# Kernel optimization log

Hardware: AMD Instinct MI355X
Metric: run time of the kernel (lower is better)

## Reference

```python
import jax, jax.numpy as jnp
import numpy as np
from jax import lax

M_POINT = 1024
NSAMPLE = 16
GRASPNESS_THRESHOLD = 0.1
HMIN, HMAX = -0.02, 0.04  # cylinder height range (GraspNet CloudCrop)
RADII = (0.025, 0.05, 0.075, 0.1)
BIG = 1e10


def _fps(xyz, mask):
    """Masked furthest point sampling. xyz [N,3], mask [N] bool -> idx [M_POINT] int32.
    Masked-out points carry -BIG min-distance so they are never selected."""
    first = jnp.argmax(mask).astype(jnp.int32)  # first graspable point (ragged FPS start)
    dists = jnp.where(mask, BIG, -BIG)
    idxs = jnp.zeros((M_POINT,), jnp.int32).at[0].set(first)

    def body(i, carry):
        idxs, dists = carry
        last = xyz[idxs[i - 1]]
        d = jnp.sum((xyz - last) ** 2, axis=-1)
        dists = jnp.where(mask, jnp.minimum(dists, d), -BIG)
        nxt = jnp.argmax(dists).astype(jnp.int32)
        return idxs.at[i].set(nxt), dists

    idxs, _ = lax.fori_loop(1, M_POINT, body, (idxs, dists))
    return idxs


def _cylinder_crop(xyz_g, feat_g, rot, radius, w1, b1, w2, b2):
    """Cylinder query + group + shared MLP + maxpool.
    xyz_g [B,M,3], feat_g [B,M,C], rot [B,M,3,3] -> [B,M,256]."""
    B, M, _ = xyz_g.shape
    # offsets of candidate n relative to seed m, expressed in the seed's gripper frame
    diff = xyz_g[:, None, :, :] - xyz_g[:, :, None, :]          # [B,M(seed),M(cand),3]
    local = jnp.einsum('bmnj,bmji->bmni', diff, rot)            # rotate into approach frame
    along = local[..., 0]
    r2 = local[..., 1] ** 2 + local[..., 2] ** 2
    cond = (r2 < radius * radius) & (along > HMIN) & (along < HMAX)  # [B,M,M]
    # first NSAMPLE in-cylinder indices (ball-query semantics: pad with first hit)
    order = jnp.where(cond, jnp.arange(M)[None, None, :], M)
    sel = jnp.argsort(order, axis=-1)[..., :NSAMPLE].astype(jnp.int32)  # [B,M,NS]
    cnt = cond.sum(axis=-1)                                     # [B,M]
    fill = sel[..., :1]
    idx = jnp.where(jnp.arange(NSAMPLE)[None, None, :] < cnt[..., None], sel, fill)
    idx = jnp.where(cnt[..., None] > 0, idx, 0)
    grouped_xyz = jnp.take_along_axis(local, idx[..., None], axis=2) / radius  # [B,M,NS,3]
    grouped_feat = feat_g[jnp.arange(B)[:, None, None], idx]                    # [B,M,NS,C]
    g = jnp.concatenate([grouped_xyz, grouped_feat], axis=-1)                   # [B,M,NS,3+C]
    h = jax.nn.relu(jnp.einsum('bmnf,of->bmno', g, w1) + b1)
    h = jax.nn.relu(jnp.einsum('bmnf,of->bmno', h, w2) + b2)
    return h.max(axis=2)                                                        # [B,M,256]


def setup_inputs() -> dict:
    key = jax.random.key(0)
    ks = jax.random.split(key, 10)
    B, N, C = 4, 20000, 512
    return {
        'seed_xyz': jax.random.normal(ks[0], (B, N, 3), jnp.float32),
        'seed_features': jax.random.normal(ks[1], (B, C, N), jnp.float32),
        'objectness_score': jax.random.normal(ks[2], (B, 2, N), jnp.float32),
        'graspness_score': jax.random.uniform(ks[3], (B, N), jnp.float32),
        'grasp_top_views_rot': jax.random.normal(ks[4], (B, M_POINT, 3, 3), jnp.float32),
        'crop_w1': jax.random.normal(ks[5], (4, 256, 3 + C), jnp.float32) * 0.05,
        'crop_b1': jnp.zeros((4, 256), jnp.float32),
        'crop_w2': jax.random.normal(ks[6], (4, 256, 256), jnp.float32) * 0.05,
        'crop_b2': jnp.zeros((4, 256), jnp.float32),
        'fuse_w': jax.random.normal(ks[7], (256, 1024), jnp.float32) * 0.05,
        'fuse_b': jnp.zeros((256,), jnp.float32),
    }


def reference(seed_xyz, seed_features, objectness_score, graspness_score,
              grasp_top_views_rot, crop_w1, crop_b1, crop_w2, crop_b2,
              fuse_w, fuse_b):
    # graspable mask (per-point, data dependent)
    objectness_mask = jnp.argmax(objectness_score, axis=1) == 1       # [B,N]
    graspness_mask = graspness_score > GRASPNESS_THRESHOLD
    graspable_mask = objectness_mask & graspness_mask
    # masked FPS per sample, then gather
    idxs = jax.vmap(_fps)(seed_xyz, graspable_mask)                    # [B,M]
    xyz_g = jnp.take_along_axis(seed_xyz, idxs[:, :, None], axis=1)    # [B,M,3]
    feat = seed_features.transpose(0, 2, 1)                            # [B,N,C]
    feat_g = jnp.take_along_axis(feat, idxs[:, :, None], axis=1)       # [B,M,C]
    # multiscale cylinder crops
    feats = [_cylinder_crop(xyz_g, feat_g, grasp_top_views_rot, RADII[k],
                            crop_w1[k], crop_b1[k], crop_w2[k], crop_b2[k])
             for k in range(4)]
    cat = jnp.concatenate(feats, axis=-1)                              # [B,M,1024]
    fused = jnp.einsum('bmf,of->bom', cat, fuse_w) + fuse_b[None, :, None]  # [B,256,M]
    return fused
```

## Files before the change

### kernel.cpp

```cpp
#include <hip/hip_runtime.h>
#include <cstdint>
#include <cfloat>
#include <climits>

#define NPTS 20000
#define NB 4
#define MP 1024
#define CF 512
#define MAXCH 20
#define KFAST 10240
#define PPAIR 10

__constant__ float c_r2[4]  = { (float)(0.025*0.025), (float)(0.05*0.05),
                                (float)(0.075*0.075), (float)(0.1*0.1) };
__constant__ float c_rad[4] = { 0.025f, 0.05f, 0.075f, 0.1f };

#define DPP_XOR1   0xB1
#define DPP_XOR2   0x4E
#define DPP_HMIRR  0x141
#define DPP_MIRR   0x140
#define DPP_BC15   0x142
#define DPP_BC31   0x143

typedef float v2f __attribute__((ext_vector_type(2)));

__device__ __forceinline__ v2f pk_add(v2f a, v2f b){
    v2f d; asm("v_pk_add_f32 %0, %1, %2" : "=v"(d) : "v"(a), "v"(b)); return d;
}
__device__ __forceinline__ v2f pk_mul(v2f a, v2f b){
    v2f d; asm("v_pk_mul_f32 %0, %1, %2" : "=v"(d) : "v"(a), "v"(b)); return d;
}

template<int CTRL>
__device__ __forceinline__ float fmax_dpp(float m)
{
    int mi = __float_as_int(m);
    int oi = __builtin_amdgcn_update_dpp(mi, mi, CTRL, 0xf, 0xf, false);
    return fmaxf(m, __int_as_float(oi));
}

template<int CTRL>
__device__ __forceinline__ unsigned long long kmax_step(unsigned long long k)
{
    unsigned int lo = (unsigned int)k;
    unsigned int hi = (unsigned int)(k >> 32);
    unsigned int olo = (unsigned int)__builtin_amdgcn_update_dpp((int)lo, (int)lo, CTRL, 0xf, 0xf, false);
    unsigned int ohi = (unsigned int)__builtin_amdgcn_update_dpp((int)hi, (int)hi, CTRL, 0xf, 0xf, false);
    unsigned long long ok = ((unsigned long long)ohi << 32) | (unsigned long long)olo;
    return (ok > k) ? ok : k;
}

__global__ __launch_bounds__(1024)
void k_fps_compact(const float* __restrict__ xyz, const float* __restrict__ obj,
                   const float* __restrict__ grasp,
                   float* __restrict__ xc, float* __restrict__ yc,
                   float* __restrict__ zc, int* __restrict__ ci,
                   int* __restrict__ kv)
{
    const int b = blockIdx.x;
    const int tid = threadIdx.x;
    const int lane = tid & 63, wid = tid >> 6;
    const float* xb  = xyz   + (size_t)b * NPTS * 3;
    const float* ob0 = obj   + (size_t)b * 2 * NPTS;
    const float* ob1 = ob0 + NPTS;
    const float* gb  = grasp + (size_t)b * NPTS;
    float* xcb = xc + (size_t)b * 20480;
    float* ycb = yc + (size_t)b * 20480;
    float* zcb = zc + (size_t)b * 20480;
    int*   cib = ci + (size_t)b * 20480;

    __shared__ int sWaveCnt[16];

    int kbase = 0;
    for (int i = 0; i < MAXCH; ++i) {
        int n = i * MP + tid;
        bool msk = false; float x = 0.f, y = 0.f, z = 0.f;
        if (n < NPTS) {
            msk = (ob1[n] > ob0[n]) && (gb[n] > 0.1f);
            if (msk) { x = xb[n*3+0]; y = xb[n*3+1]; z = xb[n*3+2]; }
        }
        unsigned long long bal = __ballot(msk);
        if (lane == 0) sWaveCnt[wid] = __popcll(bal);
        __syncthreads();
        int pre = 0, tot = 0;
        for (int w = 0; w < 16; ++w) { int c = sWaveCnt[w]; tot += c; if (w < wid) pre += c; }
        if (msk) {
            int rank = kbase + pre + __popcll(bal & ((1ull << lane) - 1ull));
            xcb[rank] = x; ycb[rank] = y; zcb[rank] = z; cib[rank] = n;
        }
        kbase += tot;
        __syncthreads();
    }
    if (tid == 0) kv[b] = kbase;
}

__global__ __launch_bounds__(512, 2)
void k_fps_loop(const float* __restrict__ xyz, const int* __restrict__ kv,
                const float* __restrict__ xc, const float* __restrict__ yc,
                const float* __restrict__ zc, const int* __restrict__ ci,
                int* __restrict__ idxs, float* __restrict__ xyz_g)
{
    const int b = blockIdx.x;
    const int tid = threadIdx.x;
    const int lane = tid & 63, wid = tid >> 6;
    const float* xb  = xyz + (size_t)b * NPTS * 3;
    const float* xcb = xc + (size_t)b * 20480;
    const float* ycb = yc + (size_t)b * 20480;
    const float* zcb = zc + (size_t)b * 20480;
    const int*   cib = ci + (size_t)b * 20480;

    __shared__ float sXYZ[3 * KFAST];
    __shared__ int   s_sel[MP];
    __shared__ unsigned long long sKy[2][8];
    __shared__ float sMax[2][8];
    __shared__ int   sWinc[2];
    float* sX = sXYZ;
    float* sY = sXYZ + KFAST;
    float* sZ = sXYZ + 2 * KFAST;

    const int K = kv[b];

    if (K == 0) {
        for (int t = tid; t < MP; t += 512) {
            idxs[b*MP + t] = 0;
            xyz_g[((size_t)b*MP + t)*3 + 0] = xb[0];
            xyz_g[((size_t)b*MP + t)*3 + 1] = xb[1];
            xyz_g[((size_t)b*MP + t)*3 + 2] = xb[2];
        }
        return;
    }

    if (K <= KFAST) {
        for (int c = tid; c < KFAST; c += 512) {
            bool v = c < K;
            sX[c] = v ? xcb[c] : 0.f;
            sY[c] = v ? ycb[c] : 0.f;
            sZ[c] = v ? zcb[c] : 0.f;
        }
        if (tid == 0) { s_sel[0] = 0; sWinc[0] = 0x7fffffff; sWinc[1] = 0x7fffffff; }
        __syncthreads();

        v2f px2[PPAIR], py2[PPAIR], pz2[PPAIR], pd2[PPAIR];
#pragma unroll
        for (int i = 0; i < PPAIR; ++i) {
            int c0 = tid + ((2*i) << 9);
            int c1 = c0 + 512;
            px2[i].x = sX[c0]; px2[i].y = sX[c1];
            py2[i].x = sY[c0]; py2[i].y = sY[c1];
            pz2[i].x = sZ[c0]; pz2[i].y = sZ[c1];
            pd2[i].x = (c0 < K) ? 1e10f : -3.0e38f;
            pd2[i].y = (c1 < K) ? 1e10f : -3.0e38f;
            asm volatile("" : "+v"(px2[i]), "+v"(py2[i]), "+v"(pz2[i]));
        }
        v2f nlx2, nly2, nlz2;
        {
            float lx = sX[0], ly = sY[0], lz = sZ[0];
            nlx2.x = nlx2.y = -lx; nly2.x = nly2.y = -ly; nlz2.x = nlz2.y = -lz;
        }

        for (int it = 1; it < MP; ++it) {
            const int p = it & 1;
#pragma unroll
            for (int i = 0; i < PPAIR; ++i) {
                v2f dx = pk_add(px2[i], nlx2);
                v2f dy = pk_add(py2[i], nly2);
                v2f dz = pk_add(pz2[i], nlz2);
                v2f s  = pk_add(pk_add(pk_mul(dx,dx), pk_mul(dy,dy)), pk_mul(dz,dz));
                pd2[i].x = fminf(pd2[i].x, s.x);
                pd2[i].y = fminf(pd2[i].y, s.y);
            }
            float q0 = fmaxf(pd2[0].x, pd2[0].y);
            float q1 = fmaxf(pd2[1].x, pd2[1].y);
            float q2 = fmaxf(pd2[2].x, pd2[2].y);
            float q3 = fmaxf(pd2[3].x, pd2[3].y);
            float q4 = fmaxf(pd2[4].x, pd2[4].y);
            float q5 = fmaxf(pd2[5].x, pd2[5].y);
            float q6 = fmaxf(pd2[6].x, pd2[6].y);
            float q7 = fmaxf(pd2[7].x, pd2[7].y);
            float q8 = fmaxf(pd2[8].x, pd2[8].y);
            float q9 = fmaxf(pd2[9].x, pd2[9].y);
            float r0 = fmaxf(fmaxf(q0, q1), fmaxf(q2, q3));
            float r1 = fmaxf(fmaxf(q4, q5), fmaxf(q6, q7));
            float bv = fmaxf(fmaxf(r0, r1), fmaxf(q8, q9));

            float wm = bv;
            wm = fmax_dpp<DPP_XOR1 >(wm);
            wm = fmax_dpp<DPP_XOR2 >(wm);
            wm = fmax_dpp<DPP_HMIRR>(wm);
            wm = fmax_dpp<DPP_MIRR >(wm);
            wm = fmax_dpp<DPP_BC15 >(wm);
            wm = fmax_dpp<DPP_BC31 >(wm);
            if (lane == 63) sMax[p][wid] = wm;
            __syncthreads();
            float g = sMax[p][lane & 7];
            g = fmax_dpp<DPP_XOR1 >(g);
            g = fmax_dpp<DPP_XOR2 >(g);
            g = fmax_dpp<DPP_HMIRR>(g);
            if (tid == 0) sWinc[p ^ 1] = 0x7fffffff;
            if (bv == g) {
                int c = 0x7fffffff;
#pragma unroll
                for (int i = PPAIR - 1; i >= 0; --i) {
                    if (pd2[i].y == g) c = tid + ((2*i+1) << 9);
                    if (pd2[i].x == g) c = tid + ((2*i  ) << 9);
                }
                atomicMin(&sWinc[p], c);
            }
            __syncthreads();
            int n = sWinc[p];
            if (tid == 0) s_sel[it] = n;
            float nx = sX[n], ny = sY[n], nz = sZ[n];
            nlx2.x = nlx2.y = -nx;
            nly2.x = nly2.y = -ny;
            nlz2.x = nlz2.y = -nz;
        }
        __syncthreads();
        for (int t = tid; t < MP; t += 512) {
            int nc = s_sel[t];
            idxs[b*MP + t] = cib[nc];
            xyz_g[((size_t)b*MP + t)*3 + 0] = sX[nc];
            xyz_g[((size_t)b*MP + t)*3 + 1] = sY[nc];
            xyz_g[((size_t)b*MP + t)*3 + 2] = sZ[nc];
        }
        return;
    }

    {
        float* fD = sXYZ;
        for (int c = tid; c < K; c += 512) fD[c] = 1e10f;
        float lx = xcb[0], ly = ycb[0], lz = zcb[0];
        if (tid == 0) s_sel[0] = 0;
        __syncthreads();
        for (int it = 1; it < MP; ++it) {
            const int p = it & 1;
            float bv = -3.4e38f; int bn = 0;
            for (int c = tid; c < K; c += 512) {
                float dx = xcb[c] - lx, dy = ycb[c] - ly, dz = zcb[c] - lz;
                float d = __fadd_rn(__fadd_rn(__fmul_rn(dx,dx), __fmul_rn(dy,dy)),
                                    __fmul_rn(dz,dz));
                float nd = fminf(fD[c], d);
                fD[c] = nd;
                bool w = nd > bv;
                bn = w ? c : bn;
                bv = fmaxf(bv, nd);
            }
            unsigned int ob = __float_as_uint(bv);
            unsigned int ord = (ob & 0x80000000u) ? ~ob : (ob | 0x80000000u);
            unsigned long long key = ((unsigned long long)ord << 32)
                                   | (unsigned int)(~bn);
            key = kmax_step<DPP_XOR1 >(key);
            key = kmax_step<DPP_XOR2 >(key);
            key = kmax_step<DPP_HMIRR>(key);
            key = kmax_step<DPP_MIRR >(key);
            key = kmax_step<DPP_BC15 >(key);
            key = kmax_step<DPP_BC31 >(key);
            if (lane == 63) sKy[p][wid] = key;
            __syncthreads();
            unsigned long long k2 = sKy[p][lane & 7];
            k2 = kmax_step<DPP_XOR1 >(k2);
            k2 = kmax_step<DPP_XOR2 >(k2);
            k2 = kmax_step<DPP_HMIRR>(k2);
            int n = ~((unsigned int)k2);
            lx = xcb[n]; ly = ycb[n]; lz = zcb[n];
            if (tid == 0) s_sel[it] = n;
        }
        __syncthreads();
        for (int t = tid; t < MP; t += 512) {
            int nc = s_sel[t];
            idxs[b*MP + t] = cib[nc];
            xyz_g[((size_t)b*MP + t)*3 + 0] = xcb[nc];
            xyz_g[((size_t)b*MP + t)*3 + 1] = ycb[nc];
            xyz_g[((size_t)b*MP + t)*3 + 2] = zcb[nc];
        }
    }
}

__global__ void k_gather_feat(const float* __restrict__ sf, const int* __restrict__ idxs,
                              float* __restrict__ feat_g)
{
    int bm = blockIdx.x;
    int b = bm >> 10;
    int n = idxs[bm];
    const float* src = sf + (size_t)b*CF*NPTS + n;
    float* dst = feat_g + (size_t)bm*CF;
    for (int c = threadIdx.x; c < CF; c += 256) dst[c] = src[(size_t)c * NPTS];
}

__global__ void k_prep(const float* __restrict__ w1, const float* __restrict__ w2,
                       float* __restrict__ w2t, float* __restrict__ w1x)
{
    int k = blockIdx.x, cb = blockIdx.y*32, ob = blockIdx.z*32;
    int tx = threadIdx.x & 31, ty = threadIdx.x >> 5;
    __shared__ float t[32][33];
    for (int r = ty; r < 32; r += 8)
        t[r][tx] = w2[((size_t)k*256 + ob + r)*256 + cb + tx];
    __syncthreads();
    for (int r = ty; r < 32; r += 8)
        w2t[((size_t)k*256 + cb + r)*256 + ob + tx] = t[tx][r];
    if (blockIdx.y == 0 && blockIdx.z == 0) {
        int o = threadIdx.x;
        for (int d = 0; d < 3; ++d)
            w1x[(k*3 + d)*256 + o] = w1[((size_t)k*256 + o)*515 + d];
    }
}

__global__ __launch_bounds__(256)
void k_f1(const float* __restrict__ feat_g, const float* __restrict__ w1,
          const float* __restrict__ b1, float* __restrict__ F1)
{
    const int rt = blockIdx.x * 64;
    const int ot = blockIdx.y * 64;
    const int k  = blockIdx.z;
    const int tid = threadIdx.x;
    __shared__ float As[16][68];
    __shared__ float Bs[16][68];
    const int lr = tid >> 2;
    const int lc = (tid & 3) * 4;
    const int tr = (tid & 15) * 4;
    const int tc = (tid >> 4) * 4;
    float acc[4][4] = {};
    for (int kk = 0; kk < CF; kk += 16) {
        const float* ap = feat_g + (size_t)(rt + lr)*CF + kk + lc;
        As[lc+0][lr] = ap[0]; As[lc+1][lr] = ap[1];
        As[lc+2][lr] = ap[2]; As[lc+3][lr] = ap[3];
        const float* bp = w1 + (size_t)(k*256 + ot + lr)*515 + 3 + kk + lc;
        Bs[lc+0][lr] = bp[0]; Bs[lc+1][lr] = bp[1];
        Bs[lc+2][lr] = bp[2]; Bs[lc+3][lr] = bp[3];
        __syncthreads();
#pragma unroll
        for (int cc = 0; cc < 16; ++cc) {
            float a0=As[cc][tr+0], a1=As[cc][tr+1], a2=As[cc][tr+2], a3=As[cc][tr+3];
            float q0=Bs[cc][tc+0], q1=Bs[cc][tc+1], q2=Bs[cc][tc+2], q3=Bs[cc][tc+3];
            acc[0][0]+=a0*q0; acc[0][1]+=a0*q1; acc[0][2]+=a0*q2; acc[0][3]+=a0*q3;
            acc[1][0]+=a1*q0; acc[1][1]+=a1*q1; acc[1][2]+=a1*q2; acc[1][3]+=a1*q3;
            acc[2][0]+=a2*q0; acc[2][1]+=a2*q1; acc[2][2]+=a2*q2; acc[2][3]+=a2*q3;
            acc[3][0]+=a3*q0; acc[3][1]+=a3*q1; acc[3][2]+=a3*q2; acc[3][3]+=a3*q3;
        }
        __syncthreads();
    }
#pragma unroll
    for (int i = 0; i < 4; ++i)
#pragma unroll
        for (int j = 0; j < 4; ++j)
            F1[((size_t)k*4096 + rt+tr+i)*256 + ot+tc+j] = acc[i][j] + b1[k*256 + ot+tc+j];
}

__global__ __launch_bounds__(1024)
void k_nbr(const float* __restrict__ xyz_g, const float* __restrict__ rot,
           int* __restrict__ sel, float* __restrict__ lxyz, int* __restrict__ cnt)
{
    const int bm = blockIdx.x;
    const int b = bm >> 10;
    const int tid = threadIdx.x;
    const int lane = tid & 63, wid = tid >> 6;
    __shared__ float sR[9], sC[3];
    __shared__ int   sSel[4][16];
    __shared__ float sL[4][16][3];
    __shared__ int   sW[16];
    __shared__ int   sCnt[4];
    __shared__ float sFb[3];
    if (tid < 9) sR[tid] = rot[(size_t)bm*9 + tid];
    if (tid < 3) sC[tid] = xyz_g[(size_t)bm*3 + tid];
    __syncthreads();
    float x = xyz_g[((size_t)b*MP + tid)*3 + 0];
    float y = xyz_g[((size_t)b*MP + tid)*3 + 1];
    float z = xyz_g[((size_t)b*MP + tid)*3 + 2];
    float dx = x - sC[0], dy = y - sC[1], dz = z - sC[2];
    float l0 = __fadd_rn(__fadd_rn(__fmul_rn(dx,sR[0]), __fmul_rn(dy,sR[3])), __fmul_rn(dz,sR[6]));
    float l1 = __fadd_rn(__fadd_rn(__fmul_rn(dx,sR[1]), __fmul_rn(dy,sR[4])), __fmul_rn(dz,sR[7]));
    float l2 = __fadd_rn(__fadd_rn(__fmul_rn(dx,sR[2]), __fmul_rn(dy,sR[5])), __fmul_rn(dz,sR[8]));
    float r2 = __fadd_rn(__fmul_rn(l1,l1), __fmul_rn(l2,l2));
    bool basec = (l0 > -0.02f) && (l0 < 0.04f);
    if (tid == 0) { sFb[0]=l0; sFb[1]=l1; sFb[2]=l2; }
    for (int k = 0; k < 4; ++k) {
        bool c = basec && (r2 < c_r2[k]);
        unsigned long long bal = __ballot(c);
        if (lane == 0) sW[wid] = __popcll(bal);
        __syncthreads();
        int pre = 0, tot = 0;
        for (int w = 0; w < 16; ++w) { int cw = sW[w]; tot += cw; if (w < wid) pre += cw; }
        int rank = pre + __popcll(bal & ((1ull << lane) - 1ull));
        if (c && rank < 16) {
            sSel[k][rank] = tid;
            sL[k][rank][0] = l0; sL[k][rank][1] = l1; sL[k][rank][2] = l2;
        }
        if (tid == 0) sCnt[k] = min(tot, 16);
        __syncthreads();
    }
    if (tid < 64) {
        int k = tid >> 4, j = tid & 15;
        int ck = sCnt[k];
        int src = (j < ck) ? j : 0;
        int v; float a0, a1, a2;
        if (ck > 0) { v = sSel[k][src]; a0=sL[k][src][0]; a1=sL[k][src][1]; a2=sL[k][src][2]; }
        else        { v = 0; a0=sFb[0]; a1=sFb[1]; a2=sFb[2]; }
        size_t off = ((size_t)bm*4 + k)*16 + j;
        sel[off] = v;
        lxyz[off*3+0]=a0; lxyz[off*3+1]=a1; lxyz[off*3+2]=a2;
        if (j == 0) cnt[bm*4 + k] = (ck > 0) ? ck : 1;
    }
}

__global__ __launch_bounds__(256)
void k_mlp(const float* __restrict__ F1, const float* __restrict__ w1x,
           const float* __restrict__ w2t, const float* __restrict__ b2,
           const int* __restrict__ sel, const float* __restrict__ lxyz,
           const int* __restrict__ cnt, float* __restrict__ cat)
{
    const int gid = blockIdx.x;
    const int k = gid & 3;
    const int g0 = (gid >> 2) * 4;
    const int o = threadIdx.x;
    __shared__ float h1s[64][256];
    int u0 = cnt[(g0+0)*4 + k], u1 = cnt[(g0+1)*4 + k],
        u2 = cnt[(g0+2)*4 + k], u3 = cnt[(g0+3)*4 + k];
    int off1 = u0, off2 = u0+u1, off3 = off2+u2, tot = off3+u3;
    const float wx0 = w1x[(k*3+0)*256 + o];
    const float wx1 = w1x[(k*3+1)*256 + o];
    const float wx2 = w1x[(k*3+2)*256 + o];
    const float rad = c_rad[k];
    const int bbase = (g0 >> 10) * MP;
    for (int r = 0; r < tot; ++r) {
        int t = (r >= off1) + (r >= off2) + (r >= off3);
        int toff = (t==0) ? 0 : ((t==1) ? off1 : ((t==2) ? off2 : off3));
        int j = r - toff;
        int bmk = (g0 + t)*4 + k;
        int n = sel[(size_t)bmk*16 + j];
        float lx = lxyz[((size_t)bmk*16 + j)*3 + 0];
        float ly = lxyz[((size_t)bmk*16 + j)*3 + 1];
        float lz = lxyz[((size_t)bmk*16 + j)*3 + 2];
        float v = F1[((size_t)k*4096 + bbase + n)*256 + o];
        v += (lx/rad)*wx0 + (ly/rad)*wx1 + (lz/rad)*wx2;
        h1s[r][o] = fmaxf(v, 0.f);
    }
    __syncthreads();
    const float b2v = b2[k*256 + o];
    float m0=0.f, m1=0.f, m2=0.f, m3=0.f;
    const float* w2c = w2t + (size_t)k*65536 + o;
    for (int base = 0; base < tot; base += 4) {
        int r0 = base;
        int r1 = min(base+1, tot-1);
        int r2 = min(base+2, tot-1);
        int r3 = min(base+3, tot-1);
        float a0=0.f, a1=0.f, a2=0.f, a3=0.f;
        for (int c = 0; c < 256; c += 4) {
            float wA = w2c[(c+0)*256], wB = w2c[(c+1)*256];
            float wC = w2c[(c+2)*256], wD = w2c[(c+3)*256];
            float4 h;
            h = *(const float4*)&h1s[r0][c]; a0 += h.x*wA + h.y*wB + h.z*wC + h.w*wD;
            h = *(const float4*)&h1s[r1][c]; a1 += h.x*wA + h.y*wB + h.z*wC + h.w*wD;
            h = *(const float4*)&h1s[r2][c]; a2 += h.x*wA + h.y*wB + h.z*wC + h.w*wD;
            h = *(const float4*)&h1s[r3][c]; a3 += h.x*wA + h.y*wB + h.z*wC + h.w*wD;
        }
#pragma unroll
        for (int q = 0; q < 4; ++q) {
            int r = base + q;
            if (r < tot) {
                float a = (q==0) ? a0 : ((q==1) ? a1 : ((q==2) ? a2 : a3));
                int t = (r >= off1) + (r >= off2) + (r >= off3);
                float val = fmaxf(a + b2v, 0.f);
                if      (t==0) m0 = fmaxf(m0, val);
                else if (t==1) m1 = fmaxf(m1, val);
                else if (t==2) m2 = fmaxf(m2, val);
                else           m3 = fmaxf(m3, val);
            }
        }
    }
    cat[(size_t)(g0+0)*1024 + k*256 + o] = m0;
    cat[(size_t)(g0+1)*1024 + k*256 + o] = m1;
    cat[(size_t)(g0+2)*1024 + k*256 + o] = m2;
    cat[(size_t)(g0+3)*1024 + k*256 + o] = m3;
}

__global__ void k_transpose(const float* __restrict__ cat, float* __restrict__ catT)
{
    int bt = blockIdx.x;
    int b = bt >> 10;
    int t2 = bt & 1023;
    int mi = (t2 >> 5) * 32, fi = (t2 & 31) * 32;
    int tx = threadIdx.x & 31, ty = threadIdx.x >> 5;
    __shared__ float t[32][33];
    const float* src = cat + (size_t)b * 1048576;
    float* dst = catT + (size_t)b * 1048576;
    for (int r = ty; r < 32; r += 8) t[r][tx] = src[(size_t)(mi + r)*1024 + fi + tx];
    __syncthreads();
    for (int r = ty; r < 32; r += 8) dst[(size_t)(fi + r)*1024 + mi + tx] = t[tx][r];
}

__global__ __launch_bounds__(256)
void k_fuse(const float* __restrict__ catT, const float* __restrict__ fw,
            const float* __restrict__ fb, float* __restrict__ out)
{
    const int o0 = blockIdx.x * 4;
    const int b = blockIdx.y;
    const int m = threadIdx.x * 4;
    const float* ct = catT + (size_t)b * 1048576 + m;
    float4 a0 = {0,0,0,0}, a1 = a0, a2 = a0, a3 = a0;
    for (int f = 0; f < 1024; ++f) {
        const float4 cv = *(const float4*)(ct + (size_t)f*1024);
        float w0 = fw[(size_t)(o0+0)*1024 + f];
        float w1 = fw[(size_t)(o0+1)*1024 + f];
        float w2 = fw[(size_t)(o0+2)*1024 + f];
        float w3 = fw[(size_t)(o0+3)*1024 + f];
        a0.x += cv.x*w0; a0.y += cv.y*w0; a0.z += cv.z*w0; a0.w += cv.w*w0;
        a1.x += cv.x*w1; a1.y += cv.y*w1; a1.z += cv.z*w1; a1.w += cv.w*w1;
        a2.x += cv.x*w2; a2.y += cv.y*w2; a2.z += cv.z*w2; a2.w += cv.w*w2;
        a3.x += cv.x*w3; a3.y += cv.y*w3; a3.z += cv.z*w3; a3.w += cv.w*w3;
    }
#pragma unroll
    for (int q = 0; q < 4; ++q) {
        float bb = fb[o0+q];
        float4 r = (q==0) ? a0 : ((q==1) ? a1 : ((q==2) ? a2 : a3));
        r.x += bb; r.y += bb; r.z += bb; r.w += bb;
        *(float4*)&out[((size_t)b*256 + o0 + q)*1024 + m] = r;
    }
}

extern "C" void kernel_launch(void* const* d_in, const int* in_sizes, int n_in,
                              void* d_out, int out_size, void* d_ws, size_t ws_size,
                              hipStream_t stream)
{
    const float* seed_xyz      = (const float*)d_in[0];
    const float* seed_features = (const float*)d_in[1];
    const float* objectness    = (const float*)d_in[2];
    const float* graspness     = (const float*)d_in[3];
    const float* rot           = (const float*)d_in[4];
    const float* w1            = (const float*)d_in[5];
    const float* b1            = (const float*)d_in[6];
    const float* w2            = (const float*)d_in[7];
    const float* b2            = (const float*)d_in[8];
    const float* fw            = (const float*)d_in[9];
    const float* fb            = (const float*)d_in[10];
    float* out = (float*)d_out;

    char* ws = (char*)d_ws;
    size_t off = 0;
    int*   idxs   = (int*)(ws + off);  off += 16u<<10;
    float* xyz_g  = (float*)(ws + off); off += 48u<<10;
    float* feat_g = (float*)(ws + off); off += 8u<<20;
    float* F1     = (float*)(ws + off); off += 16u<<20;
    float* w2t    = (float*)(ws + off); off += 1u<<20;
    float* w1x    = (float*)(ws + off); off += 64u<<10;
    int*   sel    = (int*)(ws + off);   off += 1u<<20;
    int*   cnt    = (int*)(ws + off);   off += 64u<<10;
    float* lxyz   = (float*)(ws + off); off += 3u<<20;
    float* cat    = (float*)(ws + off); off += 16u<<20;
    float* catT   = (float*)(ws + off); off += 16u<<20;

    float* xc = cat;
    float* yc = cat + 4*20480;
    float* zc = cat + 8*20480;
    int*   ci = (int*)(cat + 12*20480);
    int*   kv = (int*)((char*)w1x + 32768);

    k_fps_compact<<<NB, 1024, 0, stream>>>(seed_xyz, objectness, graspness,
                                           xc, yc, zc, ci, kv);
    k_fps_loop<<<NB, 512, 0, stream>>>(seed_xyz, kv, xc, yc, zc, ci, idxs, xyz_g);
    k_prep<<<dim3(4,8,8), 256, 0, stream>>>(w1, w2, w2t, w1x);
    k_gather_feat<<<NB*MP, 256, 0, stream>>>(seed_features, idxs, feat_g);
    k_f1<<<dim3(64,4,4), 256, 0, stream>>>(feat_g, w1, b1, F1);
    k_nbr<<<NB*MP, 1024, 0, stream>>>(xyz_g, rot, sel, lxyz, cnt);
    k_mlp<<<4096, 256, 0, stream>>>(F1, w1x, w2t, b2, sel, lxyz, cnt, cat);
    k_transpose<<<4096, 256, 0, stream>>>(cat, catT);
    k_fuse<<<dim3(64,4), 256, 0, stream>>>(catT, fw, fb, out);
}
```

Baseline: 1.771 ms.

## Shrink FPS block to 256 threads and use single-barrier packed key argmax

The FPS loop kernel now runs with 256 threads per block, each holding 40 points in registers instead of 20. The per-iteration argmax is changed from a float max reduction, a barrier and a shared atomicMin tie-break followed by a second barrier, to one packed 64-bit (distance, ~index) key reduction across lanes with one barrier; every thread then reads the four wave keys directly. This removes a barrier and the atomic from each of the 1023 sequential iterations. In exchange each thread does twice the distance work and the block has fewer waves to hide latency, with more register pressure.

```diff
diff --git a/kernel.cpp b/kernel.cpp
--- a/kernel.cpp
+++ b/kernel.cpp
@@ -9,7 +9,8 @@
 #define CF 512
 #define MAXCH 20
 #define KFAST 10240
-#define PPAIR 10
+#define THR 256
+#define PPAIR 20
 
 __constant__ float c_r2[4]  = { (float)(0.025*0.025), (float)(0.05*0.05),
                                 (float)(0.075*0.075), (float)(0.1*0.1) };
@@ -29,14 +30,6 @@
 }
 __device__ __forceinline__ v2f pk_mul(v2f a, v2f b){
     v2f d; asm("v_pk_mul_f32 %0, %1, %2" : "=v"(d) : "v"(a), "v"(b)); return d;
-}
-
-template<int CTRL>
-__device__ __forceinline__ float fmax_dpp(float m)
-{
-    int mi = __float_as_int(m);
-    int oi = __builtin_amdgcn_update_dpp(mi, mi, CTRL, 0xf, 0xf, false);
-    return fmaxf(m, __int_as_float(oi));
 }
 
 template<int CTRL>
@@ -94,7 +87,7 @@
     if (tid == 0) kv[b] = kbase;
 }
 
-__global__ __launch_bounds__(512, 2)
+__global__ __launch_bounds__(256, 1)
 void k_fps_loop(const float* __restrict__ xyz, const int* __restrict__ kv,
                 const float* __restrict__ xc, const float* __restrict__ yc,
                 const float* __restrict__ zc, const int* __restrict__ ci,
@@ -111,9 +104,7 @@
 
     __shared__ float sXYZ[3 * KFAST];
     __shared__ int   s_sel[MP];
-    __shared__ unsigned long long sKy[2][8];
-    __shared__ float sMax[2][8];
-    __shared__ int   sWinc[2];
+    __shared__ unsigned long long sKy[2][4];
     float* sX = sXYZ;
     float* sY = sXYZ + KFAST;
     float* sZ = sXYZ + 2 * KFAST;
@@ -121,7 +112,7 @@
     const int K = kv[b];
 
     if (K == 0) {
-        for (int t = tid; t < MP; t += 512) {
+        for (int t = tid; t < MP; t += THR) {
             idxs[b*MP + t] = 0;
             xyz_g[((size_t)b*MP + t)*3 + 0] = xb[0];
             xyz_g[((size_t)b*MP + t)*3 + 1] = xb[1];
@@ -131,20 +122,20 @@
     }
 
     if (K <= KFAST) {
-        for (int c = tid; c < KFAST; c += 512) {
+        for (int c = tid; c < KFAST; c += THR) {
             bool v = c < K;
             sX[c] = v ? xcb[c] : 0.f;
             sY[c] = v ? ycb[c] : 0.f;
             sZ[c] = v ? zcb[c] : 0.f;
         }
-        if (tid == 0) { s_sel[0] = 0; sWinc[0] = 0x7fffffff; sWinc[1] = 0x7fffffff; }
+        if (tid == 0) s_sel[0] = 0;
         __syncthreads();
 
         v2f px2[PPAIR], py2[PPAIR], pz2[PPAIR], pd2[PPAIR];
 #pragma unroll
         for (int i = 0; i < PPAIR; ++i) {
-            int c0 = tid + ((2*i) << 9);
-            int c1 = c0 + 512;
+            int c0 = tid + ((2*i) << 8);
+            int c1 = c0 + THR;
             px2[i].x = sX[c0]; px2[i].y = sX[c1];
             py2[i].x = sY[c0]; py2[i].y = sY[c1];
             pz2[i].x = sZ[c0]; pz2[i].y = sZ[c1];
@@ -169,45 +160,39 @@
                 pd2[i].x = fminf(pd2[i].x, s.x);
                 pd2[i].y = fminf(pd2[i].y, s.y);
             }
-            float q0 = fmaxf(pd2[0].x, pd2[0].y);
-            float q1 = fmaxf(pd2[1].x, pd2[1].y);
-            float q2 = fmaxf(pd2[2].x, pd2[2].y);
-            float q3 = fmaxf(pd2[3].x, pd2[3].y);
-            float q4 = fmaxf(pd2[4].x, pd2[4].y);
-            float q5 = fmaxf(pd2[5].x, pd2[5].y);
-            float q6 = fmaxf(pd2[6].x, pd2[6].y);
-            float q7 = fmaxf(pd2[7].x, pd2[7].y);
-            float q8 = fmaxf(pd2[8].x, pd2[8].y);
-            float q9 = fmaxf(pd2[9].x, pd2[9].y);
-            float r0 = fmaxf(fmaxf(q0, q1), fmaxf(q2, q3));
-            float r1 = fmaxf(fmaxf(q4, q5), fmaxf(q6, q7));
-            float bv = fmaxf(fmaxf(r0, r1), fmaxf(q8, q9));
-
-            float wm = bv;
-            wm = fmax_dpp<DPP_XOR1 >(wm);
-            wm = fmax_dpp<DPP_XOR2 >(wm);
-            wm = fmax_dpp<DPP_HMIRR>(wm);
-            wm = fmax_dpp<DPP_MIRR >(wm);
-            wm = fmax_dpp<DPP_BC15 >(wm);
-            wm = fmax_dpp<DPP_BC31 >(wm);
-            if (lane == 63) sMax[p][wid] = wm;
+            float q[PPAIR];
+#pragma unroll
+            for (int i = 0; i < PPAIR; ++i) q[i] = fmaxf(pd2[i].x, pd2[i].y);
+            float t0 = fmaxf(fmaxf(q[0], q[1]),  fmaxf(q[2], q[3]));
+            float t1 = fmaxf(fmaxf(q[4], q[5]),  fmaxf(q[6], q[7]));
+            float t2 = fmaxf(fmaxf(q[8], q[9]),  fmaxf(q[10], q[11]));
+            float t3 = fmaxf(fmaxf(q[12], q[13]), fmaxf(q[14], q[15]));
+            float t4 = fmaxf(fmaxf(q[16], q[17]), fmaxf(q[18], q[19]));
+            float bv = fmaxf(fmaxf(fmaxf(t0, t1), fmaxf(t2, t3)), t4);
+            int c = 0x7fffffff;
+#pragma unroll
+            for (int i = PPAIR - 1; i >= 0; --i) {
+                if (pd2[i].y == bv) c = tid + ((2*i+1) << 8);
+                if (pd2[i].x == bv) c = tid + ((2*i  ) << 8);
+            }
+            unsigned int ob = __float_as_uint(bv);
+            unsigned int ord = (ob & 0x80000000u) ? ~ob : (ob | 0x80000000u);
+            unsigned long long key = ((unsigned long long)ord << 32)
+                                   | (unsigned int)(~c);
+            key = kmax_step<DPP_XOR1 >(key);
+            key = kmax_step<DPP_XOR2 >(key);
+            key = kmax_step<DPP_HMIRR>(key);
+            key = kmax_step<DPP_MIRR >(key);
+            key = kmax_step<DPP_BC15 >(key);
+            key = kmax_step<DPP_BC31 >(key);
+            if (lane == 63) sKy[p][wid] = key;
             __syncthreads();
-            float g = sMax[p][lane & 7];
-            g = fmax_dpp<DPP_XOR1 >(g);
-            g = fmax_dpp<DPP_XOR2 >(g);
-            g = fmax_dpp<DPP_HMIRR>(g);
-            if (tid == 0) sWinc[p ^ 1] = 0x7fffffff;
-            if (bv == g) {
-                int c = 0x7fffffff;
-#pragma unroll
-                for (int i = PPAIR - 1; i >= 0; --i) {
-                    if (pd2[i].y == g) c = tid + ((2*i+1) << 9);
-                    if (pd2[i].x == g) c = tid + ((2*i  ) << 9);
-                }
-                atomicMin(&sWinc[p], c);
-            }
-            __syncthreads();
-            int n = sWinc[p];
+            unsigned long long ka = sKy[p][0], kb = sKy[p][1];
+            unsigned long long kc = sKy[p][2], kd = sKy[p][3];
+            unsigned long long m01 = (kb > ka) ? kb : ka;
+            unsigned long long m23 = (kd > kc) ? kd : kc;
+            unsigned long long km  = (m23 > m01) ? m23 : m01;
+            int n = ~((unsigned int)km);
             if (tid == 0) s_sel[it] = n;
             float nx = sX[n], ny = sY[n], nz = sZ[n];
             nlx2.x = nlx2.y = -nx;
@@ -215,7 +200,7 @@
             nlz2.x = nlz2.y = -nz;
         }
         __syncthreads();
-        for (int t = tid; t < MP; t += 512) {
+        for (int t = tid; t < MP; t += THR) {
             int nc = s_sel[t];
             idxs[b*MP + t] = cib[nc];
             xyz_g[((size_t)b*MP + t)*3 + 0] = sX[nc];
@@ -227,14 +212,14 @@
 
     {
         float* fD = sXYZ;
-        for (int c = tid; c < K; c += 512) fD[c] = 1e10f;
+        for (int c = tid; c < K; c += THR) fD[c] = 1e10f;
         float lx = xcb[0], ly = ycb[0], lz = zcb[0];
         if (tid == 0) s_sel[0] = 0;
         __syncthreads();
         for (int it = 1; it < MP; ++it) {
             const int p = it & 1;
             float bv = -3.4e38f; int bn = 0;
-            for (int c = tid; c < K; c += 512) {
+            for (int c = tid; c < K; c += THR) {
                 float dx = xcb[c] - lx, dy = ycb[c] - ly, dz = zcb[c] - lz;
                 float d = __fadd_rn(__fadd_rn(__fmul_rn(dx,dx), __fmul_rn(dy,dy)),
                                     __fmul_rn(dz,dz));
@@ -256,16 +241,17 @@
             key = kmax_step<DPP_BC31 >(key);
             if (lane == 63) sKy[p][wid] = key;
             __syncthreads();
-            unsigned long long k2 = sKy[p][lane & 7];
-            k2 = kmax_step<DPP_XOR1 >(k2);
-            k2 = kmax_step<DPP_XOR2 >(k2);
-            k2 = kmax_step<DPP_HMIRR>(k2);
-            int n = ~((unsigned int)k2);
+            unsigned long long ka = sKy[p][0], kb = sKy[p][1];
+            unsigned long long kc = sKy[p][2], kd = sKy[p][3];
+            unsigned long long m01 = (kb > ka) ? kb : ka;
+            unsigned long long m23 = (kd > kc) ? kd : kc;
+            unsigned long long km  = (m23 > m01) ? m23 : m01;
+            int n = ~((unsigned int)km);
             lx = xcb[n]; ly = ycb[n]; lz = zcb[n];
             if (tid == 0) s_sel[it] = n;
         }
         __syncthreads();
-        for (int t = tid; t < MP; t += 512) {
+        for (int t = tid; t < MP; t += THR) {
             int nc = s_sel[t];
             idxs[b*MP + t] = cib[nc];
             xyz_g[((size_t)b*MP + t)*3 + 0] = xcb[nc];
@@ -555,7 +541,7 @@
 
     k_fps_compact<<<NB, 1024, 0, stream>>>(seed_xyz, objectness, graspness,
                                            xc, yc, zc, ci, kv);
-    k_fps_loop<<<NB, 512, 0, stream>>>(seed_xyz, kv, xc, yc, zc, ci, idxs, xyz_g);
+    k_fps_loop<<<NB, THR, 0, stream>>>(seed_xyz, kv, xc, yc, zc, ci, idxs, xyz_g);
     k_prep<<<dim3(4,8,8), 256, 0, stream>>>(w1, w2, w2t, w1x);
     k_gather_feat<<<NB*MP, 256, 0, stream>>>(seed_features, idxs, feat_g);
     k_f1<<<dim3(64,4,4), 256, 0, stream>>>(feat_g, w1, b1, F1);
```

Measured after the change: 1.775 ms. No clear change (+0.2%).
